# Kernel tuning notes

Hardware: AMD Instinct MI355X
Metric: run time of the kernel (lower is better)

## Reference

```python
import jax, jax.numpy as jnp
import numpy as np

TOKENS = 512
IN_F = 8192
OUT_F = 8192
RANK = 64
NNZ = 8192
QMAX = 127.0  # int8 symmetric


def setup_inputs() -> dict:
    key = jax.random.key(0)
    ks = jax.random.split(key, 12)
    x = jax.random.normal(ks[0], (TOKENS, IN_F), dtype=jnp.float32)
    quantized_weight = jax.random.randint(ks[1], (OUT_F, IN_F), -128, 128, dtype=jnp.int32)
    weight_scale = jax.random.uniform(ks[2], (OUT_F,), minval=0.005, maxval=0.02, dtype=jnp.float32)
    smooth_scales = jax.random.uniform(ks[3], (IN_F,), minval=0.5, maxval=2.0, dtype=jnp.float32)
    act_scale = jnp.array([0.05], dtype=jnp.float32)
    outlier_rows = jax.random.randint(ks[4], (NNZ,), 0, OUT_F, dtype=jnp.int32)
    outlier_cols = jax.random.randint(ks[5], (NNZ,), 0, IN_F, dtype=jnp.int32)
    outlier_vals = jax.random.normal(ks[6], (NNZ,), dtype=jnp.float32) * 0.1
    svd_U = jax.random.normal(ks[7], (OUT_F, RANK), dtype=jnp.float32) * 0.02
    svd_S = jax.random.uniform(ks[8], (RANK,), minval=0.1, maxval=1.0, dtype=jnp.float32)
    svd_V = jax.random.normal(ks[9], (IN_F, RANK), dtype=jnp.float32) * 0.02
    bias = jax.random.normal(ks[10], (OUT_F,), dtype=jnp.float32) * 0.01
    return {"x": x, "quantized_weight": quantized_weight, "weight_scale": weight_scale,
            "smooth_scales": smooth_scales, "act_scale": act_scale,
            "outlier_rows": outlier_rows, "outlier_cols": outlier_cols,
            "outlier_vals": outlier_vals, "svd_U": svd_U, "svd_S": svd_S,
            "svd_V": svd_V, "bias": bias}


def reference(x, quantized_weight, weight_scale, smooth_scales, act_scale,
              outlier_rows, outlier_cols, outlier_vals, svd_U, svd_S, svd_V, bias):
    # SmoothQuant: migrate activation outliers into the weight scales
    x_s = x / smooth_scales  # [T, in]
    # per-tensor symmetric int8 activation fake-quant
    a = act_scale[0]
    x_q = jnp.clip(jnp.round(x_s / a), -QMAX - 1.0, QMAX)
    x_dq = x_q * a  # [T, in]
    # dequantize weight: per-output-channel scale, plus sparse outlier correction
    W = quantized_weight.astype(jnp.float32) * weight_scale[:, None]  # [out, in]
    W = W.at[outlier_rows, outlier_cols].add(outlier_vals)
    # dense quantized matmul
    y = x_dq @ W.T  # [T, out]
    # low-rank SVD residual: x @ (U S V^T)^T = ((x @ V) * S) @ U^T
    y = y + ((x_dq @ svd_V) * svd_S) @ svd_U.T
    return y + bias
```

## Files before the change

kernel.cpp:

```cpp
#include <hip/hip_runtime.h>
#include <hip/hip_bf16.h>

#define TOKENS 512
#define IN_F 8192
#define OUT_F 8192
#define RANK 64
#define NNZ 8192

#define KSPLIT 4
#define KRANGE (IN_F / KSPLIT)
#define BM 512
#define BN 64
#define BK 64
#define NT (KRANGE / BK)

typedef __attribute__((ext_vector_type(8))) short short8;
typedef __attribute__((ext_vector_type(4))) float f32x4;
typedef __attribute__((ext_vector_type(4))) int int4v;

__device__ __forceinline__ unsigned short f2bf(float f) {
  unsigned int u = __builtin_bit_cast(unsigned int, f);
  u += 0x7FFFu + ((u >> 16) & 1u);
  return (unsigned short)(u >> 16);
}
__device__ __forceinline__ float bf2f(unsigned short b) {
  unsigned int u = ((unsigned int)b) << 16;
  return __builtin_bit_cast(float, u);
}

__device__ __forceinline__ void gload_lds16(const void* g, void* l) {
  __builtin_amdgcn_global_load_lds(
      (const __attribute__((address_space(1))) unsigned int*)(g),
      (__attribute__((address_space(3))) unsigned int*)(l), 16, 0, 0);
}

#define WAIT_VM(n) asm volatile("s_waitcnt vmcnt(" #n ")" ::: "memory")
#define WAIT_LGKM0 asm volatile("s_waitcnt lgkmcnt(0)" ::: "memory")

__global__ __launch_bounds__(256) void k_quant(const float* __restrict__ x,
                                               const float* __restrict__ smooth,
                                               const float* __restrict__ act,
                                               unsigned short* __restrict__ Abf,
                                               unsigned char* __restrict__ Aq) {
  int idx = blockIdx.x * 256 + threadIdx.x;
  int base = idx * 4;
  int col = base & (IN_F - 1);
  float a = act[0];
  float4 xx = *(const float4*)(x + base);
  float4 ss = *(const float4*)(smooth + col);
  float q0 = fminf(fmaxf(rintf((xx.x / ss.x) / a), -128.f), 127.f);
  float q1 = fminf(fmaxf(rintf((xx.y / ss.y) / a), -128.f), 127.f);
  float q2 = fminf(fmaxf(rintf((xx.z / ss.z) / a), -128.f), 127.f);
  float q3 = fminf(fmaxf(rintf((xx.w / ss.w) / a), -128.f), 127.f);
  ushort4 o;
  o.x = f2bf(q0); o.y = f2bf(q1); o.z = f2bf(q2); o.w = f2bf(q3);
  *(ushort4*)(Abf + base) = o;
  int i0 = (int)q0, i1 = (int)q1, i2 = (int)q2, i3 = (int)q3;
  unsigned int p = (i0 & 0xFF) | ((i1 & 0xFF) << 8) | ((i2 & 0xFF) << 16) |
                   ((unsigned)(i3 & 0xFF) << 24);
  *(unsigned int*)(Aq + base) = p;
}

__global__ __launch_bounds__(256) void k_lr1(const unsigned short* __restrict__ Abf,
                                             const float* __restrict__ V,
                                             const float* __restrict__ S,
                                             const float* __restrict__ act,
                                             float* __restrict__ t) {
  int bid = blockIdx.x;
  int mb = (bid & 3) * 128;
  int kb0 = (bid >> 2) * 512;
  int tid = threadIdx.x, w = tid >> 6, l = tid & 63;
  int lr = l & 15, lg = l >> 4;
  f32x4 acc[2][4] = {};
  for (int ks = 0; ks < 16; ++ks) {
    int kb = kb0 + ks * 32;
    short8 af[2];
#pragma unroll
    for (int fi = 0; fi < 2; ++fi) {
      int row = mb + w * 32 + fi * 16 + lr;
      af[fi] = *(const short8*)(Abf + (size_t)row * IN_F + kb + lg * 8);
    }
    short8 bfr[4];
#pragma unroll
    for (int fj = 0; fj < 4; ++fj) {
      int rk = fj * 16 + lr;
      short8 bv;
#pragma unroll
      for (int j = 0; j < 8; ++j)
        bv[j] = (short)f2bf(V[(size_t)(kb + lg * 8 + j) * RANK + rk]);
      bfr[fj] = bv;
    }
#pragma unroll
    for (int fi = 0; fi < 2; ++fi)
#pragma unroll
      for (int fj = 0; fj < 4; ++fj)
        acc[fi][fj] = __builtin_amdgcn_mfma_f32_16x16x32_bf16(af[fi], bfr[fj], acc[fi][fj], 0, 0, 0);
  }
  float a = act[0];
#pragma unroll
  for (int fi = 0; fi < 2; ++fi)
#pragma unroll
    for (int fj = 0; fj < 4; ++fj) {
      int rk = fj * 16 + lr;
      float sc = a * S[rk];
#pragma unroll
      for (int r = 0; r < 4; ++r) {
        int tok = mb + w * 32 + fi * 16 + lg * 4 + r;
        atomicAdd(t + tok * RANK + rk, acc[fi][fj][r] * sc);
      }
    }
}

__global__ __launch_bounds__(256) void k_lr2(const float* __restrict__ t,
                                             const float* __restrict__ U,
                                             const float* __restrict__ bias,
                                             float* __restrict__ out) {
  int bid = blockIdx.x;
  int mb = (bid & 3) * 128;
  int nb = (bid >> 2) * 128;
  int tid = threadIdx.x, w = tid >> 6, l = tid & 63;
  int lr = l & 15, lg = l >> 4;
  int wm = w >> 1, wn = w & 1;
  f32x4 acc[4][4] = {};
#pragma unroll
  for (int kk = 0; kk < 2; ++kk) {
    short8 af[4], bfr[4];
#pragma unroll
    for (int fi = 0; fi < 4; ++fi) {
      int row = mb + wm * 64 + fi * 16 + lr;
      const float4* tp = (const float4*)(t + (size_t)row * RANK + kk * 32 + lg * 8);
      float4 t0 = tp[0], t1 = tp[1];
      af[fi][0] = f2bf(t0.x); af[fi][1] = f2bf(t0.y);
      af[fi][2] = f2bf(t0.z); af[fi][3] = f2bf(t0.w);
      af[fi][4] = f2bf(t1.x); af[fi][5] = f2bf(t1.y);
      af[fi][6] = f2bf(t1.z); af[fi][7] = f2bf(t1.w);
    }
#pragma unroll
    for (int fj = 0; fj < 4; ++fj) {
      int row = nb + wn * 64 + fj * 16 + lr;
      const float4* up = (const float4*)(U + (size_t)row * RANK + kk * 32 + lg * 8);
      float4 u0 = up[0], u1 = up[1];
      bfr[fj][0] = f2bf(u0.x); bfr[fj][1] = f2bf(u0.y);
      bfr[fj][2] = f2bf(u0.z); bfr[fj][3] = f2bf(u0.w);
      bfr[fj][4] = f2bf(u1.x); bfr[fj][5] = f2bf(u1.y);
      bfr[fj][6] = f2bf(u1.z); bfr[fj][7] = f2bf(u1.w);
    }
#pragma unroll
    for (int fi = 0; fi < 4; ++fi)
#pragma unroll
      for (int fj = 0; fj < 4; ++fj)
        acc[fi][fj] = __builtin_amdgcn_mfma_f32_16x16x32_bf16(af[fi], bfr[fj], acc[fi][fj], 0, 0, 0);
  }
#pragma unroll
  for (int fj = 0; fj < 4; ++fj) {
    int o = nb + wn * 64 + fj * 16 + lr;
    float b = bias[o];
#pragma unroll
    for (int fi = 0; fi < 4; ++fi)
#pragma unroll
      for (int r = 0; r < 4; ++r) {
        int tok = mb + wm * 64 + fi * 16 + lg * 4 + r;
        out[(size_t)tok * OUT_F + o] = b + acc[fi][fj][r];
      }
  }
}

__global__ __launch_bounds__(256) void k_outlier_merge(
    const unsigned short* __restrict__ Abf, const int* __restrict__ rows,
    const int* __restrict__ cols, const float* __restrict__ vals,
    const float* __restrict__ act, const float* __restrict__ wscale,
    const int* __restrict__ part, float* __restrict__ out) {
  __shared__ float accr[OUT_F];
  int tk = blockIdx.x;
  for (int i = threadIdx.x; i < OUT_F; i += 256) accr[i] = 0.f;
  __syncthreads();
  float a = act[0];
  for (int i = threadIdx.x; i < NNZ; i += 256) {
    int r = rows[i], c = cols[i];
    float v = vals[i];
    float xq = bf2f(Abf[(size_t)tk * IN_F + c]);
    atomicAdd(accr + r, a * xq * v);
  }
  __syncthreads();
  float* orow = out + (size_t)tk * OUT_F;
  const int* p0 = part + (size_t)tk * OUT_F;
  const int* p1 = p0 + (size_t)TOKENS * OUT_F;
  const int* p2 = p1 + (size_t)TOKENS * OUT_F;
  const int* p3 = p2 + (size_t)TOKENS * OUT_F;
  for (int i = threadIdx.x * 4; i < OUT_F; i += 1024) {
    int4v s0 = *(const int4v*)(p0 + i);
    int4v s1 = *(const int4v*)(p1 + i);
    int4v s2 = *(const int4v*)(p2 + i);
    int4v s3 = *(const int4v*)(p3 + i);
    float4 ws = *(const float4*)(wscale + i);
    float4 ov = *(const float4*)(orow + i);
    ov.x += accr[i + 0] + (float)(s0[0] + s1[0] + s2[0] + s3[0]) * a * ws.x;
    ov.y += accr[i + 1] + (float)(s0[1] + s1[1] + s2[1] + s3[1]) * a * ws.y;
    ov.z += accr[i + 2] + (float)(s0[2] + s1[2] + s2[2] + s3[2]) * a * ws.z;
    ov.w += accr[i + 3] + (float)(s0[3] + s1[3] + s2[3] + s3[3]) * a * ws.w;
    *(float4*)(orow + i) = ov;
  }
}

__global__ __launch_bounds__(512, 4) void k_gemm(const unsigned char* __restrict__ Aq,
                                                 const int* __restrict__ W,
                                                 int* __restrict__ part) {
  __shared__ __align__(16) unsigned char As[2][BM * BK];
  __shared__ __align__(16) unsigned char Bs[2][BN * BK];

  int d = blockIdx.x;
  int wg = (d & 7) * 64 + (d >> 3);
  int ks = wg >> 7;
  int nb = wg & 127;
  int kb0 = ks * KRANGE;

  int tid = threadIdx.x, w = tid >> 6, l = tid & 63;
  int lr = l & 15, lg = l >> 4;
  int wm = w >> 1, wn = w & 1;

  int4v acc[8][2] = {};
  int4v wa[2], wb[2];

  const int rB = tid >> 3;
  const int kcB = (tid & 7) * 8;

  auto LOAD_W = [&](int4v (&wr)[2], int kb) {
    const int* wp = W + (size_t)(nb * BN + rB) * IN_F + kb + kcB;
    wr[0] = *(const int4v*)wp;
    wr[1] = *(const int4v*)(wp + 4);
  };
  auto STAGE_A = [&](int buf, int kb) {
#pragma unroll
    for (int i = 0; i < 4; ++i) {
      int ubase = i * 512 + w * 64;
      int ell = ubase + l;
      int r = ell >> 2, up = ell & 3;
      int u = up ^ ((r >> 1) & 3);
      gload_lds16(Aq + (size_t)r * IN_F + kb + u * 16, &As[buf][(size_t)ubase * 16]);
    }
  };
  auto WRITE_B = [&](int buf, const int4v (&wr)[2]) {
    unsigned int w0 = 0, w1 = 0;
#pragma unroll
    for (int j = 0; j < 4; ++j) w0 |= ((unsigned)(wr[0][j] & 0xFF)) << (8 * j);
#pragma unroll
    for (int j = 0; j < 4; ++j) w1 |= ((unsigned)(wr[1][j] & 0xFF)) << (8 * j);
    int u = kcB >> 4, sub = (kcB >> 3) & 1;
    int us = u ^ ((rB >> 1) & 3);
    uint2 val; val.x = w0; val.y = w1;
    *(uint2*)(&Bs[buf][(size_t)rB * BK + us * 16 + sub * 8]) = val;
  };
  auto LDFA = [&](int buf, int row) -> int4v {
    int u = lg ^ ((row >> 1) & 3);
    return *(const int4v*)(&As[buf][(size_t)row * BK + u * 16]);
  };
  auto LDFB = [&](int buf, int row) -> int4v {
    int u = lg ^ ((row >> 1) & 3);
    return *(const int4v*)(&Bs[buf][(size_t)row * BK + u * 16]);
  };
  auto COMPUTE = [&](int buf) {
    __builtin_amdgcn_s_setprio(1);
    int4v b0 = LDFB(buf, wn * 32 + lr);
    int4v b1 = LDFB(buf, wn * 32 + 16 + lr);
#pragma unroll
    for (int fi = 0; fi < 8; ++fi) {
      int4v af = LDFA(buf, wm * 128 + fi * 16 + lr);
      acc[fi][0] = __builtin_amdgcn_mfma_i32_16x16x64_i8(af, b0, acc[fi][0], 0, 0, 0);
      acc[fi][1] = __builtin_amdgcn_mfma_i32_16x16x64_i8(af, b1, acc[fi][1], 0, 0, 0);
    }
    __builtin_amdgcn_s_setprio(0);
  };

  LOAD_W(wa, kb0);
  STAGE_A(0, kb0);
  WAIT_VM(4);
  WRITE_B(0, wa);
  LOAD_W(wa, kb0 + BK);
  WAIT_VM(2);
  WAIT_LGKM0;
  __builtin_amdgcn_s_barrier();

#define ITER(kt, CUR, wcur, wnxt)                                   \
  {                                                                 \
    STAGE_A(CUR ^ 1, kb0 + (((kt) + 1) & (NT - 1)) * BK);           \
    LOAD_W(wnxt, kb0 + (((kt) + 2) & (NT - 1)) * BK);               \
    COMPUTE(CUR);                                                   \
    WAIT_VM(6);                                                     \
    WRITE_B(CUR ^ 1, wcur);                                         \
    WAIT_VM(2);                                                     \
    WAIT_LGKM0;                                                     \
    __builtin_amdgcn_s_barrier();                                   \
  }

  for (int kt = 0; kt < NT; kt += 2) {
    ITER(kt, 0, wa, wb);
    ITER(kt + 1, 1, wb, wa);
  }
#undef ITER

  int* pp = part + (size_t)ks * TOKENS * OUT_F;
#pragma unroll
  for (int fj = 0; fj < 2; ++fj) {
    int o = nb * BN + wn * 32 + fj * 16 + lr;
#pragma unroll
    for (int fi = 0; fi < 8; ++fi)
#pragma unroll
      for (int rr = 0; rr < 4; ++rr) {
        int tok = wm * 128 + fi * 16 + lg * 4 + rr;
        pp[(size_t)tok * OUT_F + o] = acc[fi][fj][rr];
      }
  }
}

extern "C" void kernel_launch(void* const* d_in, const int* in_sizes, int n_in,
                              void* d_out, int out_size, void* d_ws, size_t ws_size,
                              hipStream_t stream) {
  const float* x = (const float*)d_in[0];
  const int* W = (const int*)d_in[1];
  const float* wscale = (const float*)d_in[2];
  const float* smooth = (const float*)d_in[3];
  const float* act = (const float*)d_in[4];
  const int* orow = (const int*)d_in[5];
  const int* ocol = (const int*)d_in[6];
  const float* oval = (const float*)d_in[7];
  const float* U = (const float*)d_in[8];
  const float* S = (const float*)d_in[9];
  const float* V = (const float*)d_in[10];
  const float* bias = (const float*)d_in[11];
  float* out = (float*)d_out;

  unsigned short* Abf = (unsigned short*)d_ws;
  unsigned char* Aq = (unsigned char*)d_ws + (size_t)TOKENS * IN_F * 2;
  float* t = (float*)((char*)d_ws + (size_t)TOKENS * IN_F * 3);
  int* part = (int*)((char*)d_ws + (size_t)TOKENS * IN_F * 3 + (size_t)TOKENS * RANK * 4);

  hipMemsetAsync(t, 0, TOKENS * RANK * sizeof(float), stream);
  k_quant<<<(TOKENS * IN_F / 4) / 256, 256, 0, stream>>>(x, smooth, act, Abf, Aq);
  k_gemm<<<512, 512, 0, stream>>>(Aq, W, part);
  k_lr1<<<64, 256, 0, stream>>>(Abf, V, S, act, t);
  k_lr2<<<256, 256, 0, stream>>>(t, U, bias, out);
  k_outlier_merge<<<TOKENS, 256, 0, stream>>>(Abf, orow, ocol, oval, act,
                                              wscale, part, out);
}
```

Before: 191.1 us.

## Restructure int8 GEMM: 1024-thread blocks, split-K of two, direct-register weight loads

The GEMM now uses 256 blocks of 1024 threads (16 waves) with split-K reduced from 4 to 2. A is staged into LDS in 128-wide K chunks with an XOR swizzle. Weights are loaded straight from global memory into registers and packed into int8 per wave, with no LDS stage for B. The merge kernel sums only two partials, which cuts partial-buffer traffic. The risks are un-overlapped global weight loads inside the compute loop, a full vmcnt(0) wait every chunk, and lower grid parallelism.

```diff
diff --git a/kernel.cpp b/kernel.cpp
--- a/kernel.cpp
+++ b/kernel.cpp
@@ -7,12 +7,12 @@
 #define RANK 64
 #define NNZ 8192
 
-#define KSPLIT 4
+#define KSPLIT 2
 #define KRANGE (IN_F / KSPLIT)
 #define BM 512
 #define BN 64
-#define BK 64
-#define NT (KRANGE / BK)
+#define KC 128
+#define NCH (KRANGE / KC)
 
 typedef __attribute__((ext_vector_type(8))) short short8;
 typedef __attribute__((ext_vector_type(4))) float f32x4;
@@ -34,7 +34,7 @@
       (__attribute__((address_space(3))) unsigned int*)(l), 16, 0, 0);
 }
 
-#define WAIT_VM(n) asm volatile("s_waitcnt vmcnt(" #n ")" ::: "memory")
+#define WAIT_VM0 asm volatile("s_waitcnt vmcnt(0)" ::: "memory")
 #define WAIT_LGKM0 asm volatile("s_waitcnt lgkmcnt(0)" ::: "memory")
 
 __global__ __launch_bounds__(256) void k_quant(const float* __restrict__ x,
@@ -185,128 +185,106 @@
   float* orow = out + (size_t)tk * OUT_F;
   const int* p0 = part + (size_t)tk * OUT_F;
   const int* p1 = p0 + (size_t)TOKENS * OUT_F;
-  const int* p2 = p1 + (size_t)TOKENS * OUT_F;
-  const int* p3 = p2 + (size_t)TOKENS * OUT_F;
   for (int i = threadIdx.x * 4; i < OUT_F; i += 1024) {
     int4v s0 = *(const int4v*)(p0 + i);
     int4v s1 = *(const int4v*)(p1 + i);
-    int4v s2 = *(const int4v*)(p2 + i);
-    int4v s3 = *(const int4v*)(p3 + i);
     float4 ws = *(const float4*)(wscale + i);
     float4 ov = *(const float4*)(orow + i);
-    ov.x += accr[i + 0] + (float)(s0[0] + s1[0] + s2[0] + s3[0]) * a * ws.x;
-    ov.y += accr[i + 1] + (float)(s0[1] + s1[1] + s2[1] + s3[1]) * a * ws.y;
-    ov.z += accr[i + 2] + (float)(s0[2] + s1[2] + s2[2] + s3[2]) * a * ws.z;
-    ov.w += accr[i + 3] + (float)(s0[3] + s1[3] + s2[3] + s3[3]) * a * ws.w;
+    ov.x += accr[i + 0] + (float)(s0[0] + s1[0]) * a * ws.x;
+    ov.y += accr[i + 1] + (float)(s0[1] + s1[1]) * a * ws.y;
+    ov.z += accr[i + 2] + (float)(s0[2] + s1[2]) * a * ws.z;
+    ov.w += accr[i + 3] + (float)(s0[3] + s1[3]) * a * ws.w;
     *(float4*)(orow + i) = ov;
   }
 }
 
-__global__ __launch_bounds__(512, 4) void k_gemm(const unsigned char* __restrict__ Aq,
-                                                 const int* __restrict__ W,
-                                                 int* __restrict__ part) {
-  __shared__ __align__(16) unsigned char As[2][BM * BK];
-  __shared__ __align__(16) unsigned char Bs[2][BN * BK];
+__global__ __launch_bounds__(1024, 4) void k_gemm(const unsigned char* __restrict__ Aq,
+                                                  const int* __restrict__ W,
+                                                  int* __restrict__ part) {
+  __shared__ __align__(16) unsigned char As[2][BM * KC];
 
   int d = blockIdx.x;
-  int wg = (d & 7) * 64 + (d >> 3);
-  int ks = wg >> 7;
-  int nb = wg & 127;
+  int xcd = d & 7;
+  int ks = xcd >> 2;
+  int nb = (xcd & 3) * 32 + (d >> 3);
   int kb0 = ks * KRANGE;
 
   int tid = threadIdx.x, w = tid >> 6, l = tid & 63;
   int lr = l & 15, lg = l >> 4;
   int wm = w >> 1, wn = w & 1;
 
-  int4v acc[8][2] = {};
-  int4v wa[2], wb[2];
-
-  const int rB = tid >> 3;
-  const int kcB = (tid & 7) * 8;
-
-  auto LOAD_W = [&](int4v (&wr)[2], int kb) {
-    const int* wp = W + (size_t)(nb * BN + rB) * IN_F + kb + kcB;
-    wr[0] = *(const int4v*)wp;
-    wr[1] = *(const int4v*)(wp + 4);
+  int4v acc[4][2] = {};
+
+  auto REFILL = [&](int buf, int c) {
+#pragma unroll
+    for (int i = 0; i < 4; ++i) {
+      int ubase = (i * 16 + w) * 64;
+      int U = ubase + l;
+      int r = U >> 3, u = U & 7;
+      gload_lds16(Aq + (size_t)r * IN_F + kb0 + c * KC + (u ^ (r & 7)) * 16,
+                  &As[buf][(size_t)ubase * 16]);
+    }
   };
-  auto STAGE_A = [&](int buf, int kb) {
-#pragma unroll
-    for (int i = 0; i < 4; ++i) {
-      int ubase = i * 512 + w * 64;
-      int ell = ubase + l;
-      int r = ell >> 2, up = ell & 3;
-      int u = up ^ ((r >> 1) & 3);
-      gload_lds16(Aq + (size_t)r * IN_F + kb + u * 16, &As[buf][(size_t)ubase * 16]);
-    }
+  auto LDFA = [&](int buf, int row, int u) -> int4v {
+    int us = u ^ (row & 7);
+    return *(const int4v*)(&As[buf][(size_t)row * KC + us * 16]);
   };
-  auto WRITE_B = [&](int buf, const int4v (&wr)[2]) {
-    unsigned int w0 = 0, w1 = 0;
-#pragma unroll
-    for (int j = 0; j < 4; ++j) w0 |= ((unsigned)(wr[0][j] & 0xFF)) << (8 * j);
-#pragma unroll
-    for (int j = 0; j < 4; ++j) w1 |= ((unsigned)(wr[1][j] & 0xFF)) << (8 * j);
-    int u = kcB >> 4, sub = (kcB >> 3) & 1;
-    int us = u ^ ((rB >> 1) & 3);
-    uint2 val; val.x = w0; val.y = w1;
-    *(uint2*)(&Bs[buf][(size_t)rB * BK + us * 16 + sub * 8]) = val;
+  auto LOADB = [&](int c, int ks2, int fj) -> int4v {
+    int o = nb * BN + wn * 32 + fj * 16 + lr;
+    const int* wp = W + (size_t)o * IN_F + kb0 + c * KC + ks2 * 64 + lg * 16;
+    int4v r0 = ((const int4v*)wp)[0];
+    int4v r1 = ((const int4v*)wp)[1];
+    int4v r2 = ((const int4v*)wp)[2];
+    int4v r3 = ((const int4v*)wp)[3];
+    int4v b;
+    b[0] = (r0[0] & 0xFF) | ((r0[1] & 0xFF) << 8) | ((r0[2] & 0xFF) << 16) | (r0[3] << 24);
+    b[1] = (r1[0] & 0xFF) | ((r1[1] & 0xFF) << 8) | ((r1[2] & 0xFF) << 16) | (r1[3] << 24);
+    b[2] = (r2[0] & 0xFF) | ((r2[1] & 0xFF) << 8) | ((r2[2] & 0xFF) << 16) | (r2[3] << 24);
+    b[3] = (r3[0] & 0xFF) | ((r3[1] & 0xFF) << 8) | ((r3[2] & 0xFF) << 16) | (r3[3] << 24);
+    return b;
   };
-  auto LDFA = [&](int buf, int row) -> int4v {
-    int u = lg ^ ((row >> 1) & 3);
-    return *(const int4v*)(&As[buf][(size_t)row * BK + u * 16]);
-  };
-  auto LDFB = [&](int buf, int row) -> int4v {
-    int u = lg ^ ((row >> 1) & 3);
-    return *(const int4v*)(&Bs[buf][(size_t)row * BK + u * 16]);
-  };
-  auto COMPUTE = [&](int buf) {
-    __builtin_amdgcn_s_setprio(1);
-    int4v b0 = LDFB(buf, wn * 32 + lr);
-    int4v b1 = LDFB(buf, wn * 32 + 16 + lr);
-#pragma unroll
-    for (int fi = 0; fi < 8; ++fi) {
-      int4v af = LDFA(buf, wm * 128 + fi * 16 + lr);
-      acc[fi][0] = __builtin_amdgcn_mfma_i32_16x16x64_i8(af, b0, acc[fi][0], 0, 0, 0);
-      acc[fi][1] = __builtin_amdgcn_mfma_i32_16x16x64_i8(af, b1, acc[fi][1], 0, 0, 0);
-    }
-    __builtin_amdgcn_s_setprio(0);
-  };
-
-  LOAD_W(wa, kb0);
-  STAGE_A(0, kb0);
-  WAIT_VM(4);
-  WRITE_B(0, wa);
-  LOAD_W(wa, kb0 + BK);
-  WAIT_VM(2);
-  WAIT_LGKM0;
+
+  REFILL(0, 0);
+  WAIT_VM0;
   __builtin_amdgcn_s_barrier();
 
-#define ITER(kt, CUR, wcur, wnxt)                                   \
-  {                                                                 \
-    STAGE_A(CUR ^ 1, kb0 + (((kt) + 1) & (NT - 1)) * BK);           \
-    LOAD_W(wnxt, kb0 + (((kt) + 2) & (NT - 1)) * BK);               \
-    COMPUTE(CUR);                                                   \
-    WAIT_VM(6);                                                     \
-    WRITE_B(CUR ^ 1, wcur);                                         \
-    WAIT_VM(2);                                                     \
-    WAIT_LGKM0;                                                     \
-    __builtin_amdgcn_s_barrier();                                   \
-  }
-
-  for (int kt = 0; kt < NT; kt += 2) {
-    ITER(kt, 0, wa, wb);
-    ITER(kt + 1, 1, wb, wa);
-  }
-#undef ITER
+  for (int c = 0; c < NCH; ++c) {
+    int cur = c & 1;
+    if (c + 1 < NCH) REFILL(cur ^ 1, c + 1);
+#pragma unroll
+    for (int ks2 = 0; ks2 < 2; ++ks2) {
+      int4v b0 = LOADB(c, ks2, 0);
+      int4v b1 = LOADB(c, ks2, 1);
+      int u = ks2 * 4 + lg;
+      int4v a0 = LDFA(cur, wm * 64 + 0 * 16 + lr, u);
+      int4v a1 = LDFA(cur, wm * 64 + 1 * 16 + lr, u);
+      int4v a2 = LDFA(cur, wm * 64 + 2 * 16 + lr, u);
+      int4v a3 = LDFA(cur, wm * 64 + 3 * 16 + lr, u);
+      __builtin_amdgcn_s_setprio(1);
+      acc[0][0] = __builtin_amdgcn_mfma_i32_16x16x64_i8(a0, b0, acc[0][0], 0, 0, 0);
+      acc[1][0] = __builtin_amdgcn_mfma_i32_16x16x64_i8(a1, b0, acc[1][0], 0, 0, 0);
+      acc[2][0] = __builtin_amdgcn_mfma_i32_16x16x64_i8(a2, b0, acc[2][0], 0, 0, 0);
+      acc[3][0] = __builtin_amdgcn_mfma_i32_16x16x64_i8(a3, b0, acc[3][0], 0, 0, 0);
+      acc[0][1] = __builtin_amdgcn_mfma_i32_16x16x64_i8(a0, b1, acc[0][1], 0, 0, 0);
+      acc[1][1] = __builtin_amdgcn_mfma_i32_16x16x64_i8(a1, b1, acc[1][1], 0, 0, 0);
+      acc[2][1] = __builtin_amdgcn_mfma_i32_16x16x64_i8(a2, b1, acc[2][1], 0, 0, 0);
+      acc[3][1] = __builtin_amdgcn_mfma_i32_16x16x64_i8(a3, b1, acc[3][1], 0, 0, 0);
+      __builtin_amdgcn_s_setprio(0);
+    }
+    WAIT_VM0;
+    WAIT_LGKM0;
+    __builtin_amdgcn_s_barrier();
+  }
 
   int* pp = part + (size_t)ks * TOKENS * OUT_F;
 #pragma unroll
   for (int fj = 0; fj < 2; ++fj) {
     int o = nb * BN + wn * 32 + fj * 16 + lr;
 #pragma unroll
-    for (int fi = 0; fi < 8; ++fi)
+    for (int fi = 0; fi < 4; ++fi)
 #pragma unroll
       for (int rr = 0; rr < 4; ++rr) {
-        int tok = wm * 128 + fi * 16 + lg * 4 + rr;
+        int tok = wm * 64 + fi * 16 + lg * 4 + rr;
         pp[(size_t)tok * OUT_F + o] = acc[fi][fj][rr];
       }
   }
@@ -336,7 +314,7 @@
 
   hipMemsetAsync(t, 0, TOKENS * RANK * sizeof(float), stream);
   k_quant<<<(TOKENS * IN_F / 4) / 256, 256, 0, stream>>>(x, smooth, act, Abf, Aq);
-  k_gemm<<<512, 512, 0, stream>>>(Aq, W, part);
+  k_gemm<<<256, 1024, 0, stream>>>(Aq, W, part);
   k_lr1<<<64, 256, 0, stream>>>(Abf, V, S, act, t);
   k_lr2<<<256, 256, 0, stream>>>(t, U, bias, out);
   k_outlier_merge<<<TOKENS, 256, 0, stream>>>(Abf, orow, ocol, oval, act,
```

Measured after the change: 350.3 us. +83.3%, slower.

## Double GEMM workgroup size to 1024 threads and drop low-rank atomics

Applied to the files above, without the earlier changes.

The int8 GEMM workgroup grows from 8 to 16 waves. Each wave now owns 64 token rows instead of 128, which halves per-wave accumulators and per-thread W loads, and the vmcnt waits are adjusted to match. The low-rank first stage now writes per-K-split partial results to separate buffers instead of using atomicAdd, so the memset goes away and k_lr2 sums the 16 partials. The trade-offs are more workspace and more reads in k_lr2, and 1024-thread blocks with launch bounds (1024,8) may limit register allocation and occupancy.

```diff
diff --git a/kernel.cpp b/kernel.cpp
--- a/kernel.cpp
+++ b/kernel.cpp
@@ -13,6 +13,7 @@
 #define BN 64
 #define BK 64
 #define NT (KRANGE / BK)
+#define LRSPLIT 16
 
 typedef __attribute__((ext_vector_type(8))) short short8;
 typedef __attribute__((ext_vector_type(4))) float f32x4;
@@ -68,7 +69,8 @@
                                              float* __restrict__ t) {
   int bid = blockIdx.x;
   int mb = (bid & 3) * 128;
-  int kb0 = (bid >> 2) * 512;
+  int ksp = bid >> 2;
+  int kb0 = ksp * 512;
   int tid = threadIdx.x, w = tid >> 6, l = tid & 63;
   int lr = l & 15, lg = l >> 4;
   f32x4 acc[2][4] = {};
@@ -97,6 +99,7 @@
         acc[fi][fj] = __builtin_amdgcn_mfma_f32_16x16x32_bf16(af[fi], bfr[fj], acc[fi][fj], 0, 0, 0);
   }
   float a = act[0];
+  float* tk = t + (size_t)ksp * TOKENS * RANK;
 #pragma unroll
   for (int fi = 0; fi < 2; ++fi)
 #pragma unroll
@@ -106,7 +109,7 @@
 #pragma unroll
       for (int r = 0; r < 4; ++r) {
         int tok = mb + w * 32 + fi * 16 + lg * 4 + r;
-        atomicAdd(t + tok * RANK + rk, acc[fi][fj][r] * sc);
+        tk[(size_t)tok * RANK + rk] = acc[fi][fj][r] * sc;
       }
     }
 }
@@ -128,8 +131,14 @@
 #pragma unroll
     for (int fi = 0; fi < 4; ++fi) {
       int row = mb + wm * 64 + fi * 16 + lr;
-      const float4* tp = (const float4*)(t + (size_t)row * RANK + kk * 32 + lg * 8);
-      float4 t0 = tp[0], t1 = tp[1];
+      size_t off = (size_t)row * RANK + kk * 32 + lg * 8;
+      float4 t0 = {0, 0, 0, 0}, t1 = {0, 0, 0, 0};
+      for (int s = 0; s < LRSPLIT; ++s) {
+        const float4* tp = (const float4*)(t + (size_t)s * TOKENS * RANK + off);
+        float4 u0 = tp[0], u1 = tp[1];
+        t0.x += u0.x; t0.y += u0.y; t0.z += u0.z; t0.w += u0.w;
+        t1.x += u1.x; t1.y += u1.y; t1.z += u1.z; t1.w += u1.w;
+      }
       af[fi][0] = f2bf(t0.x); af[fi][1] = f2bf(t0.y);
       af[fi][2] = f2bf(t0.z); af[fi][3] = f2bf(t0.w);
       af[fi][4] = f2bf(t1.x); af[fi][5] = f2bf(t1.y);
@@ -202,9 +211,9 @@
   }
 }
 
-__global__ __launch_bounds__(512, 4) void k_gemm(const unsigned char* __restrict__ Aq,
-                                                 const int* __restrict__ W,
-                                                 int* __restrict__ part) {
+__global__ __launch_bounds__(1024, 8) void k_gemm(const unsigned char* __restrict__ Aq,
+                                                  const int* __restrict__ W,
+                                                  int* __restrict__ part) {
   __shared__ __align__(16) unsigned char As[2][BM * BK];
   __shared__ __align__(16) unsigned char Bs[2][BN * BK];
 
@@ -218,37 +227,32 @@
   int lr = l & 15, lg = l >> 4;
   int wm = w >> 1, wn = w & 1;
 
-  int4v acc[8][2] = {};
-  int4v wa[2], wb[2];
-
-  const int rB = tid >> 3;
-  const int kcB = (tid & 7) * 8;
-
-  auto LOAD_W = [&](int4v (&wr)[2], int kb) {
-    const int* wp = W + (size_t)(nb * BN + rB) * IN_F + kb + kcB;
-    wr[0] = *(const int4v*)wp;
-    wr[1] = *(const int4v*)(wp + 4);
+  int4v acc[4][2] = {};
+  int4v wa, wb;
+
+  const int rW = tid >> 4;
+  const int kcW = (tid & 15) * 4;
+
+  auto LOAD_W = [&](int4v& wr, int kb) {
+    wr = *(const int4v*)(W + (size_t)(nb * BN + rW) * IN_F + kb + kcW);
   };
   auto STAGE_A = [&](int buf, int kb) {
 #pragma unroll
-    for (int i = 0; i < 4; ++i) {
-      int ubase = i * 512 + w * 64;
-      int ell = ubase + l;
-      int r = ell >> 2, up = ell & 3;
+    for (int i = 0; i < 2; ++i) {
+      int ubase = i * 1024 + w * 64;
+      int U = ubase + l;
+      int r = U >> 2, up = U & 3;
       int u = up ^ ((r >> 1) & 3);
       gload_lds16(Aq + (size_t)r * IN_F + kb + u * 16, &As[buf][(size_t)ubase * 16]);
     }
   };
-  auto WRITE_B = [&](int buf, const int4v (&wr)[2]) {
-    unsigned int w0 = 0, w1 = 0;
-#pragma unroll
-    for (int j = 0; j < 4; ++j) w0 |= ((unsigned)(wr[0][j] & 0xFF)) << (8 * j);
-#pragma unroll
-    for (int j = 0; j < 4; ++j) w1 |= ((unsigned)(wr[1][j] & 0xFF)) << (8 * j);
-    int u = kcB >> 4, sub = (kcB >> 3) & 1;
-    int us = u ^ ((rB >> 1) & 3);
-    uint2 val; val.x = w0; val.y = w1;
-    *(uint2*)(&Bs[buf][(size_t)rB * BK + us * 16 + sub * 8]) = val;
+  auto WRITE_B = [&](int buf, int4v wr) {
+    unsigned int w0 = 0;
+#pragma unroll
+    for (int j = 0; j < 4; ++j) w0 |= ((unsigned)(wr[j] & 0xFF)) << (8 * j);
+    int u = kcW >> 4, rem = kcW & 15;
+    int us = u ^ ((rW >> 1) & 3);
+    *(unsigned int*)(&Bs[buf][(size_t)rW * BK + us * 16 + rem]) = w0;
   };
   auto LDFA = [&](int buf, int row) -> int4v {
     int u = lg ^ ((row >> 1) & 3);
@@ -263,8 +267,8 @@
     int4v b0 = LDFB(buf, wn * 32 + lr);
     int4v b1 = LDFB(buf, wn * 32 + 16 + lr);
 #pragma unroll
-    for (int fi = 0; fi < 8; ++fi) {
-      int4v af = LDFA(buf, wm * 128 + fi * 16 + lr);
+    for (int fi = 0; fi < 4; ++fi) {
+      int4v af = LDFA(buf, wm * 64 + fi * 16 + lr);
       acc[fi][0] = __builtin_amdgcn_mfma_i32_16x16x64_i8(af, b0, acc[fi][0], 0, 0, 0);
       acc[fi][1] = __builtin_amdgcn_mfma_i32_16x16x64_i8(af, b1, acc[fi][1], 0, 0, 0);
     }
@@ -273,10 +277,10 @@
 
   LOAD_W(wa, kb0);
   STAGE_A(0, kb0);
-  WAIT_VM(4);
+  WAIT_VM(2);
   WRITE_B(0, wa);
   LOAD_W(wa, kb0 + BK);
-  WAIT_VM(2);
+  WAIT_VM(1);
   WAIT_LGKM0;
   __builtin_amdgcn_s_barrier();
 
@@ -285,9 +289,9 @@
     STAGE_A(CUR ^ 1, kb0 + (((kt) + 1) & (NT - 1)) * BK);           \
     LOAD_W(wnxt, kb0 + (((kt) + 2) & (NT - 1)) * BK);               \
     COMPUTE(CUR);                                                   \
-    WAIT_VM(6);                                                     \
+    WAIT_VM(3);                                                     \
     WRITE_B(CUR ^ 1, wcur);                                         \
-    WAIT_VM(2);                                                     \
+    WAIT_VM(1);                                                     \
     WAIT_LGKM0;                                                     \
     __builtin_amdgcn_s_barrier();                                   \
   }
@@ -303,10 +307,10 @@
   for (int fj = 0; fj < 2; ++fj) {
     int o = nb * BN + wn * 32 + fj * 16 + lr;
 #pragma unroll
-    for (int fi = 0; fi < 8; ++fi)
+    for (int fi = 0; fi < 4; ++fi)
 #pragma unroll
       for (int rr = 0; rr < 4; ++rr) {
-        int tok = wm * 128 + fi * 16 + lg * 4 + rr;
+        int tok = wm * 64 + fi * 16 + lg * 4 + rr;
         pp[(size_t)tok * OUT_F + o] = acc[fi][fj][rr];
       }
   }
@@ -332,11 +336,11 @@
   unsigned short* Abf = (unsigned short*)d_ws;
   unsigned char* Aq = (unsigned char*)d_ws + (size_t)TOKENS * IN_F * 2;
   float* t = (float*)((char*)d_ws + (size_t)TOKENS * IN_F * 3);
-  int* part = (int*)((char*)d_ws + (size_t)TOKENS * IN_F * 3 + (size_t)TOKENS * RANK * 4);
-
-  hipMemsetAsync(t, 0, TOKENS * RANK * sizeof(float), stream);
+  int* part = (int*)((char*)d_ws + (size_t)TOKENS * IN_F * 3 +
+                     (size_t)LRSPLIT * TOKENS * RANK * 4);
+
   k_quant<<<(TOKENS * IN_F / 4) / 256, 256, 0, stream>>>(x, smooth, act, Abf, Aq);
-  k_gemm<<<512, 512, 0, stream>>>(Aq, W, part);
+  k_gemm<<<512, 1024, 0, stream>>>(Aq, W, part);
   k_lr1<<<64, 256, 0, stream>>>(Abf, V, S, act, t);
   k_lr2<<<256, 256, 0, stream>>>(t, U, bias, out);
   k_outlier_merge<<<TOKENS, 256, 0, stream>>>(Abf, orow, ocol, oval, act,
```

Result: slower. 229.7 us (+20.2%).

## Restructure int8 GEMM into 1024-thread, six-stage K32 pipeline with split barriers

Applied to the files above, without the earlier changes.

Rewrites the int8 MFMA GEMM mainloop to use 1024 threads (16 waves) with a 32-byte K-slice per stage and a six-deep ring of LDS buffers. Each 64-wide MFMA step reads two consecutive 32-byte stages, picked by lane group. Fragment loads, the barrier, and the next stage's A-to-LDS and W global loads are ordered explicitly with sched_barrier. The goal is deeper prefetch and more waves to hide the global-memory latency of the int32 weight stream. In exchange there are two barriers per iteration and smaller per-wave tiles, so each wave does less MFMA work per sync.

```diff
diff --git a/kernel.cpp b/kernel.cpp
--- a/kernel.cpp
+++ b/kernel.cpp
@@ -11,12 +11,12 @@
 #define KRANGE (IN_F / KSPLIT)
 #define BM 512
 #define BN 64
-#define BK 64
-#define NT (KRANGE / BK)
+#define NT 32
 
 typedef __attribute__((ext_vector_type(8))) short short8;
 typedef __attribute__((ext_vector_type(4))) float f32x4;
 typedef __attribute__((ext_vector_type(4))) int int4v;
+typedef __attribute__((ext_vector_type(2))) int int2v;
 
 __device__ __forceinline__ unsigned short f2bf(float f) {
   unsigned int u = __builtin_bit_cast(unsigned int, f);
@@ -36,6 +36,7 @@
 
 #define WAIT_VM(n) asm volatile("s_waitcnt vmcnt(" #n ")" ::: "memory")
 #define WAIT_LGKM0 asm volatile("s_waitcnt lgkmcnt(0)" ::: "memory")
+#define SCHED0 __builtin_amdgcn_sched_barrier(0)
 
 __global__ __launch_bounds__(256) void k_quant(const float* __restrict__ x,
                                                const float* __restrict__ smooth,
@@ -202,11 +203,11 @@
   }
 }
 
-__global__ __launch_bounds__(512, 4) void k_gemm(const unsigned char* __restrict__ Aq,
-                                                 const int* __restrict__ W,
-                                                 int* __restrict__ part) {
-  __shared__ __align__(16) unsigned char As[2][BM * BK];
-  __shared__ __align__(16) unsigned char Bs[2][BN * BK];
+__global__ __launch_bounds__(1024, 4) void k_gemm(const unsigned char* __restrict__ Aq,
+                                                  const int* __restrict__ W,
+                                                  int* __restrict__ part) {
+  __shared__ __align__(16) unsigned char As[6][512 * 32];
+  __shared__ __align__(16) unsigned char Bs[6][64 * 32];
 
   int d = blockIdx.x;
   int wg = (d & 7) * 64 + (d >> 3);
@@ -218,95 +219,107 @@
   int lr = l & 15, lg = l >> 4;
   int wm = w >> 1, wn = w & 1;
 
-  int4v acc[8][2] = {};
-  int4v wa[2], wb[2];
-
-  const int rB = tid >> 3;
-  const int kcB = (tid & 7) * 8;
-
-  auto LOAD_W = [&](int4v (&wr)[2], int kb) {
-    const int* wp = W + (size_t)(nb * BN + rB) * IN_F + kb + kcB;
-    wr[0] = *(const int4v*)wp;
-    wr[1] = *(const int4v*)(wp + 4);
-  };
-  auto STAGE_A = [&](int buf, int kb) {
-#pragma unroll
-    for (int i = 0; i < 4; ++i) {
-      int ubase = i * 512 + w * 64;
-      int ell = ubase + l;
-      int r = ell >> 2, up = ell & 3;
-      int u = up ^ ((r >> 1) & 3);
-      gload_lds16(Aq + (size_t)r * IN_F + kb + u * 16, &As[buf][(size_t)ubase * 16]);
-    }
-  };
-  auto WRITE_B = [&](int buf, const int4v (&wr)[2]) {
-    unsigned int w0 = 0, w1 = 0;
-#pragma unroll
-    for (int j = 0; j < 4; ++j) w0 |= ((unsigned)(wr[0][j] & 0xFF)) << (8 * j);
-#pragma unroll
-    for (int j = 0; j < 4; ++j) w1 |= ((unsigned)(wr[1][j] & 0xFF)) << (8 * j);
-    int u = kcB >> 4, sub = (kcB >> 3) & 1;
-    int us = u ^ ((rB >> 1) & 3);
-    uint2 val; val.x = w0; val.y = w1;
-    *(uint2*)(&Bs[buf][(size_t)rB * BK + us * 16 + sub * 8]) = val;
+  int4v acc[4][2] = {};
+  int2v ws0, ws1;
+
+  const int rA = tid >> 1, uA = tid & 1;
+  const int usA = uA ^ ((rA >> 2) & 1);
+  const int rW = tid >> 4, kcW = (tid & 15) * 2;
+  const int usW = (kcW >> 4) ^ ((rW >> 2) & 1);
+  const int offW = kcW & 15;
+
+  auto STAGE_A = [&](int buf, int h) {
+    gload_lds16(Aq + (size_t)rA * IN_F + kb0 + ((h * 32) & (KRANGE - 1)) + usA * 16,
+                &As[buf][(size_t)(w * 64) * 16]);
+  };
+  auto LOAD_W = [&](int2v& wr, int h) {
+    wr = *(const int2v*)(W + (size_t)(nb * BN + rW) * IN_F + kb0 +
+                         ((h * 32) & (KRANGE - 1)) + kcW);
+  };
+  auto DSWRITE_B = [&](int buf, int2v wr) {
+    unsigned short v = (unsigned short)((wr[0] & 0xFF) | ((wr[1] & 0xFF) << 8));
+    *(unsigned short*)(&Bs[buf][rW * 32 + usW * 16 + offW]) = v;
   };
   auto LDFA = [&](int buf, int row) -> int4v {
-    int u = lg ^ ((row >> 1) & 3);
-    return *(const int4v*)(&As[buf][(size_t)row * BK + u * 16]);
+    int us = (lg & 1) ^ ((row >> 2) & 1);
+    return *(const int4v*)(&As[buf][(size_t)row * 32 + us * 16]);
   };
   auto LDFB = [&](int buf, int row) -> int4v {
-    int u = lg ^ ((row >> 1) & 3);
-    return *(const int4v*)(&Bs[buf][(size_t)row * BK + u * 16]);
-  };
-  auto COMPUTE = [&](int buf) {
+    int us = (lg & 1) ^ ((row >> 2) & 1);
+    return *(const int4v*)(&Bs[buf][(size_t)row * 32 + us * 16]);
+  };
+
+  STAGE_A(0, 0); LOAD_W(ws0, 0);
+  STAGE_A(1, 1); LOAD_W(ws1, 1);
+  WAIT_VM(2); DSWRITE_B(0, ws0);
+  WAIT_VM(0); DSWRITE_B(1, ws1);
+  STAGE_A(2, 2); LOAD_W(ws0, 2);
+  STAGE_A(3, 3); LOAD_W(ws1, 3);
+  WAIT_VM(2); DSWRITE_B(2, ws0);
+  WAIT_VM(0); DSWRITE_B(3, ws1);
+  STAGE_A(4, 4); LOAD_W(ws0, 4);
+  STAGE_A(5, 5); LOAD_W(ws1, 5);
+  WAIT_LGKM0;
+  SCHED0;
+  __builtin_amdgcn_s_barrier();
+  SCHED0;
+
+  int c0 = 0;
+  for (int t = 0; t < NT; ++t) {
+    int c1 = c0 + 1;
+    int w4 = c0 >= 2 ? c0 - 2 : c0 + 4;
+    int w5 = w4 + 1;
+    int bufsel = lg >> 1;
+    int bA = bufsel ? c1 : c0;
+
+    int4v af0 = LDFA(bA, wm * 64 + 0 * 16 + lr);
+    int4v af1 = LDFA(bA, wm * 64 + 1 * 16 + lr);
+    int4v af2 = LDFA(bA, wm * 64 + 2 * 16 + lr);
+    int4v af3 = LDFA(bA, wm * 64 + 3 * 16 + lr);
+    int4v b0 = LDFB(bA, wn * 32 + lr);
+    int4v b1 = LDFB(bA, wn * 32 + 16 + lr);
+    WAIT_LGKM0;
+    SCHED0;
+    __builtin_amdgcn_s_barrier();
+    SCHED0;
+
+    WAIT_VM(2);
+    DSWRITE_B(w4, ws0);
+    STAGE_A(c0, 2 * t + 6);
+    LOAD_W(ws0, 2 * t + 6);
+
     __builtin_amdgcn_s_setprio(1);
-    int4v b0 = LDFB(buf, wn * 32 + lr);
-    int4v b1 = LDFB(buf, wn * 32 + 16 + lr);
-#pragma unroll
-    for (int fi = 0; fi < 8; ++fi) {
-      int4v af = LDFA(buf, wm * 128 + fi * 16 + lr);
-      acc[fi][0] = __builtin_amdgcn_mfma_i32_16x16x64_i8(af, b0, acc[fi][0], 0, 0, 0);
-      acc[fi][1] = __builtin_amdgcn_mfma_i32_16x16x64_i8(af, b1, acc[fi][1], 0, 0, 0);
-    }
+    acc[0][0] = __builtin_amdgcn_mfma_i32_16x16x64_i8(af0, b0, acc[0][0], 0, 0, 0);
+    acc[1][0] = __builtin_amdgcn_mfma_i32_16x16x64_i8(af1, b0, acc[1][0], 0, 0, 0);
+    acc[2][0] = __builtin_amdgcn_mfma_i32_16x16x64_i8(af2, b0, acc[2][0], 0, 0, 0);
+    acc[3][0] = __builtin_amdgcn_mfma_i32_16x16x64_i8(af3, b0, acc[3][0], 0, 0, 0);
+    acc[0][1] = __builtin_amdgcn_mfma_i32_16x16x64_i8(af0, b1, acc[0][1], 0, 0, 0);
+    acc[1][1] = __builtin_amdgcn_mfma_i32_16x16x64_i8(af1, b1, acc[1][1], 0, 0, 0);
+    acc[2][1] = __builtin_amdgcn_mfma_i32_16x16x64_i8(af2, b1, acc[2][1], 0, 0, 0);
+    acc[3][1] = __builtin_amdgcn_mfma_i32_16x16x64_i8(af3, b1, acc[3][1], 0, 0, 0);
     __builtin_amdgcn_s_setprio(0);
-  };
-
-  LOAD_W(wa, kb0);
-  STAGE_A(0, kb0);
-  WAIT_VM(4);
-  WRITE_B(0, wa);
-  LOAD_W(wa, kb0 + BK);
-  WAIT_VM(2);
-  WAIT_LGKM0;
-  __builtin_amdgcn_s_barrier();
-
-#define ITER(kt, CUR, wcur, wnxt)                                   \
-  {                                                                 \
-    STAGE_A(CUR ^ 1, kb0 + (((kt) + 1) & (NT - 1)) * BK);           \
-    LOAD_W(wnxt, kb0 + (((kt) + 2) & (NT - 1)) * BK);               \
-    COMPUTE(CUR);                                                   \
-    WAIT_VM(6);                                                     \
-    WRITE_B(CUR ^ 1, wcur);                                         \
-    WAIT_VM(2);                                                     \
-    WAIT_LGKM0;                                                     \
-    __builtin_amdgcn_s_barrier();                                   \
-  }
-
-  for (int kt = 0; kt < NT; kt += 2) {
-    ITER(kt, 0, wa, wb);
-    ITER(kt + 1, 1, wb, wa);
-  }
-#undef ITER
+
+    WAIT_VM(2);
+    DSWRITE_B(w5, ws1);
+    STAGE_A(c1, 2 * t + 7);
+    LOAD_W(ws1, 2 * t + 7);
+    WAIT_LGKM0;
+    SCHED0;
+    __builtin_amdgcn_s_barrier();
+    SCHED0;
+
+    c0 = c0 >= 4 ? 0 : c0 + 2;
+  }
 
   int* pp = part + (size_t)ks * TOKENS * OUT_F;
 #pragma unroll
   for (int fj = 0; fj < 2; ++fj) {
     int o = nb * BN + wn * 32 + fj * 16 + lr;
 #pragma unroll
-    for (int fi = 0; fi < 8; ++fi)
+    for (int fi = 0; fi < 4; ++fi)
 #pragma unroll
       for (int rr = 0; rr < 4; ++rr) {
-        int tok = wm * 128 + fi * 16 + lg * 4 + rr;
+        int tok = wm * 64 + fi * 16 + lg * 4 + rr;
         pp[(size_t)tok * OUT_F + o] = acc[fi][fj][rr];
       }
   }
@@ -332,11 +345,12 @@
   unsigned short* Abf = (unsigned short*)d_ws;
   unsigned char* Aq = (unsigned char*)d_ws + (size_t)TOKENS * IN_F * 2;
   float* t = (float*)((char*)d_ws + (size_t)TOKENS * IN_F * 3);
-  int* part = (int*)((char*)d_ws + (size_t)TOKENS * IN_F * 3 + (size_t)TOKENS * RANK * 4);
+  int* part = (int*)((char*)d_ws + (size_t)TOKENS * IN_F * 3 +
+                     (size_t)TOKENS * RANK * 4);
 
   hipMemsetAsync(t, 0, TOKENS * RANK * sizeof(float), stream);
   k_quant<<<(TOKENS * IN_F / 4) / 256, 256, 0, stream>>>(x, smooth, act, Abf, Aq);
-  k_gemm<<<512, 512, 0, stream>>>(Aq, W, part);
+  k_gemm<<<512, 1024, 0, stream>>>(Aq, W, part);
   k_lr1<<<64, 256, 0, stream>>>(Abf, V, S, act, t);
   k_lr2<<<256, 256, 0, stream>>>(t, U, bias, out);
   k_outlier_merge<<<TOKENS, 256, 0, stream>>>(Abf, orow, ocol, oval, act,
```

New measurement: 254.3 us. 33.1% more time.
